# Kernel tuning notes

Hardware: AMD Instinct MI355X
Metric: run time of the kernel (lower is better)

## Reference

```python
import jax, jax.numpy as jnp
import numpy as np

B, N, S, D = 8, 325, 64, 256
H = 8
HD = D // H  # head_dim = 32


def setup_inputs() -> dict:
    key = jax.random.key(0)
    ks = jax.random.split(key, 5)
    x = jax.random.normal(ks[0], (B, N, S, D), dtype=jnp.float32)
    # nn.Linear params: weight [out, in], bias [out]
    w_qkv = jax.random.normal(ks[1], (3 * D, D), dtype=jnp.float32) * (1.0 / np.sqrt(D))
    b_qkv = jax.random.normal(ks[2], (3 * D,), dtype=jnp.float32) * 0.01
    w_proj = jax.random.normal(ks[3], (D, D), dtype=jnp.float32) * (1.0 / np.sqrt(D))
    b_proj = jax.random.normal(ks[4], (D,), dtype=jnp.float32) * 0.01
    return {"x": x, "w_qkv": w_qkv, "b_qkv": b_qkv, "w_proj": w_proj, "b_proj": b_proj}


def reference(x, w_qkv, b_qkv, w_proj, b_proj):
    b, n, s, d = x.shape
    scale = (d // H) ** -0.5
    xf = x.reshape(b * n, s, d)                              # [BN, S, D]
    qkv = jnp.einsum('bsd,ed->bse', xf, w_qkv) + b_qkv       # [BN, S, 3D]
    qkv = qkv.reshape(b * n, s, 3, H, HD)
    qkv = jnp.transpose(qkv, (2, 0, 3, 1, 4))                # [3, BN, H, S, HD]
    q, k, v = qkv[0], qkv[1], qkv[2]
    attn = jnp.einsum('bhqe,bhke->bhqk', q, k) * scale       # [BN, H, S, S]
    attn = jax.nn.softmax(attn, axis=-1)
    out = jnp.einsum('bhqk,bhke->bhqe', attn, v)             # [BN, H, S, HD]
    out = jnp.transpose(out, (0, 2, 1, 3)).reshape(b * n, s, d)
    out = jnp.einsum('bsd,ed->bse', out, w_proj) + b_proj
    return out.reshape(b, n, s, d)
```

## Files before the change

### kernel.cpp

```cpp
#include <hip/hip_runtime.h>
#include <hip/hip_bf16.h>


namespace {

constexpr int S_LEN = 64;
constexpr int DM    = 256;
constexpr int SD    = S_LEN * DM;
constexpr int QKV_UNITS = 8 * 768 * 4;

typedef float f32x4 __attribute__((ext_vector_type(4)));
typedef short s16x8 __attribute__((ext_vector_type(8)));

union BF2 { __hip_bfloat162 h; unsigned u; };
__device__ __forceinline__ unsigned pkbf2(float a, float b) {
  float2 t; t.x = a; t.y = b;
  BF2 cv; cv.h = __float22bfloat162_rn(t);
  return cv.u;
}

__device__ __forceinline__ void bar_lgkm() {
  asm volatile("s_waitcnt lgkmcnt(0)" ::: "memory");
  __builtin_amdgcn_sched_barrier(0);
  __builtin_amdgcn_s_barrier();
  __builtin_amdgcn_sched_barrier(0);
}

__device__ __forceinline__ s16x8 xpose_frag(f32x4 a0, f32x4 a1, int c, int g) {
  const int src0 = ((g & 1) << 5) + c;
  const int src1 = src0 + 16;
  unsigned p00 = pkbf2(a0[0], a0[1]);
  unsigned p01 = pkbf2(a0[2], a0[3]);
  unsigned p10 = pkbf2(a1[0], a1[1]);
  unsigned p11 = pkbf2(a1[2], a1[3]);
  const bool hi = (g & 2) != 0;
  unsigned w0a = (unsigned)__shfl((int)p00, src0);
  unsigned w0b = (unsigned)__shfl((int)p10, src0);
  unsigned w1a = (unsigned)__shfl((int)p01, src0);
  unsigned w1b = (unsigned)__shfl((int)p11, src0);
  unsigned w2a = (unsigned)__shfl((int)p00, src1);
  unsigned w2b = (unsigned)__shfl((int)p10, src1);
  unsigned w3a = (unsigned)__shfl((int)p01, src1);
  unsigned w3b = (unsigned)__shfl((int)p11, src1);
  union { s16x8 v; unsigned u[4]; } r;
  r.u[0] = hi ? w0b : w0a;
  r.u[1] = hi ? w1b : w1a;
  r.u[2] = hi ? w2b : w2a;
  r.u[3] = hi ? w3b : w3a;
  return r.v;
}

__device__ __forceinline__ int wswz(int row, int u) {
  return row * 32 + ((u ^ ((row >> 1) & 3)) << 3);
}

}

__global__ void ta_prep_weights(const float* __restrict__ wqkv,
                                const float* __restrict__ wproj,
                                unsigned short* __restrict__ wsb) {
  const int o = blockIdx.x * 256 + (int)threadIdx.x;
  const float* src;
  if (o < QKV_UNITS) {
    const int ks = o / 3072, rem = o - ks * 3072;
    const int row = rem >> 2, u = rem & 3;
    const int s = (row >> 1) & 3;
    src = wqkv + row * 256 + ks * 32 + ((u ^ s) << 3);
  } else {
    const int p = o - QKV_UNITS;
    const int ks = p >> 10, rem = p & 1023;
    const int row = rem >> 2, u = rem & 3;
    const int s = (row >> 1) & 3;
    src = wproj + row * 256 + ks * 32 + ((u ^ s) << 3);
  }
  f32x4 a = *(const f32x4*)src;
  f32x4 b = *(const f32x4*)(src + 4);
  *(uint4*)(wsb + (size_t)o * 8) =
      make_uint4(pkbf2(a[0], a[1]), pkbf2(a[2], a[3]),
                 pkbf2(b[0], b[1]), pkbf2(b[2], b[3]));
}

__global__ void __launch_bounds__(512, 2)
ta_fused_kernel(const float* __restrict__ x,
                const unsigned short* __restrict__ wqt,
                const float* __restrict__ bqkv,
                const unsigned short* __restrict__ wpt,
                const float* __restrict__ bproj,
                float* __restrict__ out)
{
  __shared__ __align__(16) unsigned short lds[40960];

  const int bn = blockIdx.x;
  const int tid = (int)threadIdx.x;
  const int w = tid >> 6;
  const int l = tid & 63;
  const int g = l >> 4;
  const int c = l & 15;
  const int c7s = (c & 7) << 3;
  const int h = w;

  unsigned short* __restrict__ xls = lds;
  unsigned short* __restrict__ wb  = lds + 16384;

  const float* __restrict__ xb = x + (size_t)bn * SD;

#pragma unroll
  for (int i = 0; i < 6; ++i) {
    const int n = i * 512 + tid;
    __builtin_amdgcn_global_load_lds(
        (const __attribute__((address_space(1))) unsigned int*)(wqt + (size_t)n * 8),
        (__attribute__((address_space(3))) unsigned int*)(wb + n * 8), 16, 0, 0);
  }

#pragma unroll
  for (int it = 0; it < 4; ++it) {
    const int e = (it * 512 + tid) * 8;
    const int row = e >> 8;
    f32x4 a = __builtin_nontemporal_load((const f32x4*)(xb + e));
    f32x4 b = __builtin_nontemporal_load((const f32x4*)(xb + e + 4));
    union { s16x8 v; unsigned u[4]; } r;
    r.u[0] = pkbf2(a[0], a[1]); r.u[1] = pkbf2(a[2], a[3]);
    r.u[2] = pkbf2(b[0], b[1]); r.u[3] = pkbf2(b[2], b[3]);
    *(s16x8*)&xls[e ^ ((row & 7) << 3)] = r.v;
  }
  __syncthreads();

  f32x4 aq[2][4], ak[2][4], av[4][2];
#pragma unroll
  for (int t = 0; t < 2; ++t)
#pragma unroll
    for (int nj = 0; nj < 4; ++nj) {
      aq[t][nj] = f32x4{0.f, 0.f, 0.f, 0.f};
      ak[t][nj] = f32x4{0.f, 0.f, 0.f, 0.f};
    }
#pragma unroll
  for (int mt = 0; mt < 4; ++mt)
#pragma unroll
    for (int t = 0; t < 2; ++t) av[mt][t] = f32x4{0.f, 0.f, 0.f, 0.f};

#pragma unroll
  for (int ks = 0; ks < 8; ++ks) {
    s16x8 awq[2], awk[2], awv[2];
#pragma unroll
    for (int t = 0; t < 2; ++t) {
      awq[t] = *(const s16x8*)&wb[wswz((2 * h + t) * 16 + c, g)];
      awk[t] = *(const s16x8*)&wb[wswz(256 + 32 * h + 16 * t + c, g)];
      awv[t] = *(const s16x8*)&wb[wswz(512 + 32 * h + 16 * t + c, g)];
    }
    bar_lgkm();
    if (ks < 7) {
#pragma unroll
      for (int i = 0; i < 6; ++i) {
        const int n = i * 512 + tid;
        __builtin_amdgcn_global_load_lds(
            (const __attribute__((address_space(1))) unsigned int*)(wqt + (size_t)((ks + 1) * 3072 + n) * 8),
            (__attribute__((address_space(3))) unsigned int*)(wb + n * 8), 16, 0, 0);
      }
    }
    const int kof = ks * 32 + g * 8;
    s16x8 bx[4];
#pragma unroll
    for (int nj = 0; nj < 4; ++nj) {
      const int row = 16 * nj + c;
      bx[nj] = *(const s16x8*)&xls[(row * 256 + kof) ^ c7s];
    }
#pragma unroll
    for (int t = 0; t < 2; ++t)
#pragma unroll
      for (int nj = 0; nj < 4; ++nj) {
        aq[t][nj] = __builtin_amdgcn_mfma_f32_16x16x32_bf16(awq[t], bx[nj], aq[t][nj], 0, 0, 0);
        ak[t][nj] = __builtin_amdgcn_mfma_f32_16x16x32_bf16(awk[t], bx[nj], ak[t][nj], 0, 0, 0);
        av[nj][t] = __builtin_amdgcn_mfma_f32_16x16x32_bf16(bx[nj], awv[t], av[nj][t], 0, 0, 0);
      }
    __syncthreads();
  }

#pragma unroll
  for (int i = 0; i < 2; ++i) {
    const int n = i * 512 + tid;
    __builtin_amdgcn_global_load_lds(
        (const __attribute__((address_space(1))) unsigned int*)(wpt + (size_t)n * 8),
        (__attribute__((address_space(3))) unsigned int*)(wb + n * 8), 16, 0, 0);
  }

#pragma unroll
  for (int t = 0; t < 2; ++t) {
    f32x4 bq = *(const f32x4*)(bqkv + (2 * h + t) * 16 + 4 * g);
    f32x4 bk = *(const f32x4*)(bqkv + 256 + 32 * h + 16 * t + 4 * g);
#pragma unroll
    for (int nj = 0; nj < 4; ++nj) {
      aq[t][nj] += bq;
      ak[t][nj] += bk;
    }
  }
  {
    const float bv0 = bqkv[512 + 32 * h + c];
    const float bv1 = bqkv[512 + 32 * h + 16 + c];
#pragma unroll
    for (int mt = 0; mt < 4; ++mt)
#pragma unroll
      for (int r = 0; r < 4; ++r) {
        av[mt][0][r] += bv0;
        av[mt][1][r] += bv1;
      }
  }

  s16x8 qa[4], ka[4];
#pragma unroll
  for (int i = 0; i < 4; ++i) {
    qa[i] = xpose_frag(aq[0][i], aq[1][i], c, g);
    ka[i] = xpose_frag(ak[0][i], ak[1][i], c, g);
  }

  f32x4 sa[4][4];
#pragma unroll
  for (int ki = 0; ki < 4; ++ki)
#pragma unroll
    for (int qi = 0; qi < 4; ++qi) {
      f32x4 z = f32x4{0.f, 0.f, 0.f, 0.f};
      sa[ki][qi] = __builtin_amdgcn_mfma_f32_16x16x32_bf16(ka[ki], qa[qi], z, 0, 0, 0);
    }

  const float sc = 0.17677669529663687f * 1.4426950408889634f;
  float inv[4];
#pragma unroll
  for (int qi = 0; qi < 4; ++qi) {
    float m = sa[0][qi][0];
#pragma unroll
    for (int ki = 0; ki < 4; ++ki)
#pragma unroll
      for (int r = 0; r < 4; ++r) m = fmaxf(m, sa[ki][qi][r]);
    m = fmaxf(m, __shfl_xor(m, 16));
    m = fmaxf(m, __shfl_xor(m, 32));
    float s = 0.0f;
#pragma unroll
    for (int ki = 0; ki < 4; ++ki)
#pragma unroll
      for (int r = 0; r < 4; ++r) {
        float pv = exp2f((sa[ki][qi][r] - m) * sc);
        sa[ki][qi][r] = pv;
        s += pv;
      }
    s += __shfl_xor(s, 16);
    s += __shfl_xor(s, 32);
    inv[qi] = 1.0f / s;
  }

  s16x8 pa[4][2];
#pragma unroll
  for (int mi = 0; mi < 4; ++mi) {
    const float iv = inv[mi];
#pragma unroll
    for (int ks2 = 0; ks2 < 2; ++ks2) {
      f32x4 v0 = sa[2 * ks2][mi] * iv;
      f32x4 v1 = sa[2 * ks2 + 1][mi] * iv;
      pa[mi][ks2] = xpose_frag(v0, v1, c, g);
    }
  }

  s16x8 vb[2][2];
#pragma unroll
  for (int nd = 0; nd < 2; ++nd)
#pragma unroll
    for (int ks2 = 0; ks2 < 2; ++ks2)
      vb[nd][ks2] = xpose_frag(av[2 * ks2][nd], av[2 * ks2 + 1][nd], c, g);

  f32x4 oa[4][2];
#pragma unroll
  for (int mi = 0; mi < 4; ++mi)
#pragma unroll
    for (int nd = 0; nd < 2; ++nd) oa[mi][nd] = f32x4{0.f, 0.f, 0.f, 0.f};
#pragma unroll
  for (int ks2 = 0; ks2 < 2; ++ks2)
#pragma unroll
    for (int mi = 0; mi < 4; ++mi)
#pragma unroll
      for (int nd = 0; nd < 2; ++nd)
        oa[mi][nd] = __builtin_amdgcn_mfma_f32_16x16x32_bf16(pa[mi][ks2], vb[nd][ks2], oa[mi][nd], 0, 0, 0);

  unsigned obp[4][2][2];
#pragma unroll
  for (int mi = 0; mi < 4; ++mi)
#pragma unroll
    for (int nd = 0; nd < 2; ++nd) {
      obp[mi][nd][0] = pkbf2(oa[mi][nd][0], oa[mi][nd][1]);
      obp[mi][nd][1] = pkbf2(oa[mi][nd][2], oa[mi][nd][3]);
    }

#pragma unroll
  for (int mi = 0; mi < 4; ++mi)
#pragma unroll
    for (int nd = 0; nd < 2; ++nd)
#pragma unroll
      for (int r = 0; r < 4; ++r) {
        const int q = 16 * mi + 4 * g + r;
        const int feat = h * 32 + 16 * nd + c;
        unsigned val = obp[mi][nd][r >> 1] >> (16 * (r & 1));
        xls[(q * 256 + feat) ^ ((q & 7) << 3)] = (unsigned short)val;
      }
  __syncthreads();

  f32x4 pacc[2][4];
#pragma unroll
  for (int ti = 0; ti < 2; ++ti)
#pragma unroll
    for (int nj = 0; nj < 4; ++nj) pacc[ti][nj] = f32x4{0.f, 0.f, 0.f, 0.f};

#pragma unroll
  for (int ks = 0; ks < 8; ++ks) {
    s16x8 aw[2];
#pragma unroll
    for (int ti = 0; ti < 2; ++ti)
      aw[ti] = *(const s16x8*)&wb[wswz((2 * w + ti) * 16 + c, g)];
    bar_lgkm();
    if (ks < 7) {
#pragma unroll
      for (int i = 0; i < 2; ++i) {
        const int n = i * 512 + tid;
        __builtin_amdgcn_global_load_lds(
            (const __attribute__((address_space(1))) unsigned int*)(wpt + (size_t)((ks + 1) * 1024 + n) * 8),
            (__attribute__((address_space(3))) unsigned int*)(wb + n * 8), 16, 0, 0);
      }
    }
    const int kof = ks * 32 + 8 * g;
    s16x8 bx[4];
#pragma unroll
    for (int nj = 0; nj < 4; ++nj) {
      const int row = 16 * nj + c;
      bx[nj] = *(const s16x8*)&xls[(row * 256 + kof) ^ c7s];
    }
#pragma unroll
    for (int ti = 0; ti < 2; ++ti)
#pragma unroll
      for (int nj = 0; nj < 4; ++nj)
        pacc[ti][nj] = __builtin_amdgcn_mfma_f32_16x16x32_bf16(aw[ti], bx[nj], pacc[ti][nj], 0, 0, 0);
    __syncthreads();
  }

  float* ldsf = (float*)wb;
  float* __restrict__ ob = out + (size_t)bn * SD;
#pragma unroll
  for (int H = 0; H < 2; ++H) {
#pragma unroll
    for (int ti = 0; ti < 2; ++ti) {
      const int e0 = (2 * w + ti) * 16 + 4 * g;
      f32x4 bp = *(const f32x4*)(bproj + e0);
#pragma unroll
      for (int nj = 2 * H; nj < 2 * H + 2; ++nj) {
        const int lr = 16 * (nj - 2 * H) + c;
        f32x4 v;
        v[0] = pacc[ti][nj][0] + bp[0];
        v[1] = pacc[ti][nj][1] + bp[1];
        v[2] = pacc[ti][nj][2] + bp[2];
        v[3] = pacc[ti][nj][3] + bp[3];
        *(f32x4*)&ldsf[(lr * 256 + e0) ^ ((lr & 7) << 2)] = v;
      }
    }
    bar_lgkm();
#pragma unroll
    for (int it = 0; it < 4; ++it) {
      const int i = (it * 512 + tid) * 4;
      const int lr = i >> 8;
      f32x4 v = *(const f32x4*)&ldsf[i ^ ((lr & 7) << 2)];
      __builtin_nontemporal_store(v, (f32x4*)(ob + H * 8192 + i));
    }
    if (H == 0) bar_lgkm();
  }
}

extern "C" void kernel_launch(void* const* d_in, const int* in_sizes, int n_in,
                              void* d_out, int out_size, void* d_ws, size_t ws_size,
                              hipStream_t stream) {
  (void)n_in; (void)ws_size; (void)out_size;
  const float* x     = (const float*)d_in[0];
  const float* wqkv  = (const float*)d_in[1];
  const float* bqkv  = (const float*)d_in[2];
  const float* wproj = (const float*)d_in[3];
  const float* bproj = (const float*)d_in[4];
  float* out = (float*)d_out;

  unsigned short* wsb = (unsigned short*)d_ws;
  const unsigned short* wqt = wsb;
  const unsigned short* wpt = wsb + QKV_UNITS * 8;

  hipLaunchKernelGGL(ta_prep_weights, dim3(128), dim3(256), 0, stream, wqkv, wproj, wsb);

  const int bn_total = in_sizes[0] / SD;
  hipLaunchKernelGGL(ta_fused_kernel, dim3(bn_total), dim3(512), 0, stream,
                     x, wqt, bqkv, wpt, bproj, out);
}
```

Before: 253.0 us.

## Load V weights directly from global memory and vectorize attention output stores

The V-projection weights are no longer staged through LDS. Each wave reads its own head's bf16 V rows straight from global memory (an L2-resident row-major copy made by the prep kernel). This cuts per-step LDS staging from six to four chunks and lowers the LDS footprint, which may help occupancy. The attention-output MFMA is also transposed so each lane writes packed 64-bit values to LDS instead of scalar 16-bit stores. In exchange, the V fragment loads now pay global-memory latency inside the K loop.

Result: slower. 266.2 us (+5.2%).

```diff
diff --git a/kernel.cpp b/kernel.cpp
--- a/kernel.cpp
+++ b/kernel.cpp
@@ -7,7 +7,8 @@
 constexpr int S_LEN = 64;
 constexpr int DM    = 256;
 constexpr int SD    = S_LEN * DM;
-constexpr int QKV_UNITS = 8 * 768 * 4;
+constexpr int QK_UNITS = 8 * 512 * 4;
+constexpr int WP_UNITS = 8 * 256 * 4;
 
 typedef float f32x4 __attribute__((ext_vector_type(4)));
 typedef short s16x8 __attribute__((ext_vector_type(8)));
@@ -61,17 +62,22 @@
                                 unsigned short* __restrict__ wsb) {
   const int o = blockIdx.x * 256 + (int)threadIdx.x;
   const float* src;
-  if (o < QKV_UNITS) {
-    const int ks = o / 3072, rem = o - ks * 3072;
+  if (o < QK_UNITS) {
+    const int ks = o >> 11, rem = o & 2047;
     const int row = rem >> 2, u = rem & 3;
     const int s = (row >> 1) & 3;
     src = wqkv + row * 256 + ks * 32 + ((u ^ s) << 3);
-  } else {
-    const int p = o - QKV_UNITS;
+  } else if (o < QK_UNITS + WP_UNITS) {
+    const int p = o - QK_UNITS;
     const int ks = p >> 10, rem = p & 1023;
     const int row = rem >> 2, u = rem & 3;
     const int s = (row >> 1) & 3;
     src = wproj + row * 256 + ks * 32 + ((u ^ s) << 3);
+  } else {
+    const int p = o - (QK_UNITS + WP_UNITS);
+    const int r = p >> 5;
+    const int col = (p & 31) * 8;
+    src = wqkv + (512 + r) * 256 + col;
   }
   f32x4 a = *(const f32x4*)src;
   f32x4 b = *(const f32x4*)(src + 4);
@@ -82,13 +88,14 @@
 
 __global__ void __launch_bounds__(512, 2)
 ta_fused_kernel(const float* __restrict__ x,
-                const unsigned short* __restrict__ wqt,
+                const unsigned short* __restrict__ wqk,
                 const float* __restrict__ bqkv,
                 const unsigned short* __restrict__ wpt,
+                const unsigned short* __restrict__ wv_bf,
                 const float* __restrict__ bproj,
                 float* __restrict__ out)
 {
-  __shared__ __align__(16) unsigned short lds[40960];
+  __shared__ __align__(16) unsigned short lds[32768];
 
   const int bn = blockIdx.x;
   const int tid = (int)threadIdx.x;
@@ -105,10 +112,10 @@
   const float* __restrict__ xb = x + (size_t)bn * SD;
 
 #pragma unroll
-  for (int i = 0; i < 6; ++i) {
+  for (int i = 0; i < 4; ++i) {
     const int n = i * 512 + tid;
     __builtin_amdgcn_global_load_lds(
-        (const __attribute__((address_space(1))) unsigned int*)(wqt + (size_t)n * 8),
+        (const __attribute__((address_space(1))) unsigned int*)(wqk + (size_t)n * 8),
         (__attribute__((address_space(3))) unsigned int*)(wb + n * 8), 16, 0, 0);
   }
 
@@ -140,24 +147,27 @@
 
 #pragma unroll
   for (int ks = 0; ks < 8; ++ks) {
-    s16x8 awq[2], awk[2], awv[2];
+    s16x8 awq[2], awk[2];
 #pragma unroll
     for (int t = 0; t < 2; ++t) {
       awq[t] = *(const s16x8*)&wb[wswz((2 * h + t) * 16 + c, g)];
       awk[t] = *(const s16x8*)&wb[wswz(256 + 32 * h + 16 * t + c, g)];
-      awv[t] = *(const s16x8*)&wb[wswz(512 + 32 * h + 16 * t + c, g)];
     }
     bar_lgkm();
     if (ks < 7) {
 #pragma unroll
-      for (int i = 0; i < 6; ++i) {
+      for (int i = 0; i < 4; ++i) {
         const int n = i * 512 + tid;
         __builtin_amdgcn_global_load_lds(
-            (const __attribute__((address_space(1))) unsigned int*)(wqt + (size_t)((ks + 1) * 3072 + n) * 8),
+            (const __attribute__((address_space(1))) unsigned int*)(wqk + (size_t)((ks + 1) * 2048 + n) * 8),
             (__attribute__((address_space(3))) unsigned int*)(wb + n * 8), 16, 0, 0);
       }
     }
     const int kof = ks * 32 + g * 8;
+    s16x8 awv[2];
+#pragma unroll
+    for (int t = 0; t < 2; ++t)
+      awv[t] = *(const s16x8*)&wv_bf[(size_t)(32 * h + 16 * t + c) * 256 + kof];
     s16x8 bx[4];
 #pragma unroll
     for (int nj = 0; nj < 4; ++nj) {
@@ -265,39 +275,36 @@
     for (int ks2 = 0; ks2 < 2; ++ks2)
       vb[nd][ks2] = xpose_frag(av[2 * ks2][nd], av[2 * ks2 + 1][nd], c, g);
 
-  f32x4 oa[4][2];
-#pragma unroll
-  for (int mi = 0; mi < 4; ++mi)
-#pragma unroll
-    for (int nd = 0; nd < 2; ++nd) oa[mi][nd] = f32x4{0.f, 0.f, 0.f, 0.f};
+  f32x4 ot[2][4];
+#pragma unroll
+  for (int nd = 0; nd < 2; ++nd)
+#pragma unroll
+    for (int mi = 0; mi < 4; ++mi) ot[nd][mi] = f32x4{0.f, 0.f, 0.f, 0.f};
 #pragma unroll
   for (int ks2 = 0; ks2 < 2; ++ks2)
 #pragma unroll
-    for (int mi = 0; mi < 4; ++mi)
-#pragma unroll
-      for (int nd = 0; nd < 2; ++nd)
-        oa[mi][nd] = __builtin_amdgcn_mfma_f32_16x16x32_bf16(pa[mi][ks2], vb[nd][ks2], oa[mi][nd], 0, 0, 0);
-
-  unsigned obp[4][2][2];
-#pragma unroll
-  for (int mi = 0; mi < 4; ++mi)
-#pragma unroll
-    for (int nd = 0; nd < 2; ++nd) {
-      obp[mi][nd][0] = pkbf2(oa[mi][nd][0], oa[mi][nd][1]);
-      obp[mi][nd][1] = pkbf2(oa[mi][nd][2], oa[mi][nd][3]);
-    }
-
-#pragma unroll
-  for (int mi = 0; mi < 4; ++mi)
-#pragma unroll
     for (int nd = 0; nd < 2; ++nd)
 #pragma unroll
-      for (int r = 0; r < 4; ++r) {
-        const int q = 16 * mi + 4 * g + r;
-        const int feat = h * 32 + 16 * nd + c;
-        unsigned val = obp[mi][nd][r >> 1] >> (16 * (r & 1));
-        xls[(q * 256 + feat) ^ ((q & 7) << 3)] = (unsigned short)val;
-      }
+      for (int mi = 0; mi < 4; ++mi)
+        ot[nd][mi] = __builtin_amdgcn_mfma_f32_16x16x32_bf16(vb[nd][ks2], pa[mi][ks2], ot[nd][mi], 0, 0, 0);
+
+  uint2 obp[2][4];
+#pragma unroll
+  for (int nd = 0; nd < 2; ++nd)
+#pragma unroll
+    for (int mi = 0; mi < 4; ++mi) {
+      obp[nd][mi].x = pkbf2(ot[nd][mi][0], ot[nd][mi][1]);
+      obp[nd][mi].y = pkbf2(ot[nd][mi][2], ot[nd][mi][3]);
+    }
+
+#pragma unroll
+  for (int nd = 0; nd < 2; ++nd)
+#pragma unroll
+    for (int mi = 0; mi < 4; ++mi) {
+      const int q = 16 * mi + c;
+      const int feat = h * 32 + 16 * nd + 4 * g;
+      *(uint2*)&xls[(q * 256 + feat) ^ c7s] = obp[nd][mi];
+    }
   __syncthreads();
 
   f32x4 pacc[2][4];
@@ -380,12 +387,13 @@
   float* out = (float*)d_out;
 
   unsigned short* wsb = (unsigned short*)d_ws;
-  const unsigned short* wqt = wsb;
-  const unsigned short* wpt = wsb + QKV_UNITS * 8;
+  const unsigned short* wqk   = wsb;
+  const unsigned short* wpt   = wsb + (size_t)QK_UNITS * 8;
+  const unsigned short* wv_bf = wsb + (size_t)(QK_UNITS + WP_UNITS) * 8;
 
   hipLaunchKernelGGL(ta_prep_weights, dim3(128), dim3(256), 0, stream, wqkv, wproj, wsb);
 
   const int bn_total = in_sizes[0] / SD;
   hipLaunchKernelGGL(ta_fused_kernel, dim3(bn_total), dim3(512), 0, stream,
-                     x, wqt, bqkv, wpt, bproj, out);
-}
+                     x, wqk, bqkv, wpt, wv_bf, bproj, out);
+}
```
